# Kernel tuning notes

Measured on AMD Instinct MI355X. Metric: run time of the kernel, lower is better.

The kernel has to match this reference:

```python
import jax, jax.numpy as jnp
import numpy as np

B, ES, HS, NL, NOUT, T = 16384, 64, 64, 3, 2, 128


def setup_inputs() -> dict:
    key = jax.random.key(0)
    ks = jax.random.split(key, 9)
    k = 1.0 / np.sqrt(HS)
    u = lambda kk, shape: jax.random.uniform(kk, shape, jnp.float32, -k, k)
    return {
        "agentFutureTrajEnc": jax.random.normal(ks[0], (B, ES), jnp.float32),
        "emb_w": u(ks[1], (ES, ES)),
        "emb_b": u(ks[2], (ES,)),
        "w_ih": u(ks[3], (NL, 3 * HS, ES)),
        "w_hh": u(ks[4], (NL, 3 * HS, HS)),
        "b_ih": u(ks[5], (NL, 3 * HS)),
        "b_hh": u(ks[6], (NL, 3 * HS)),
        "out_w": u(ks[7], (NOUT, HS)),
        "out_b": u(ks[8], (NOUT,)),
        "target_length": T,
        "batch_size": B,
    }


def _gru_cell(x, h, Wi, Wh, bi, bh):
    # PyTorch GRU cell math: gates ordered (r, z, n)
    gi = x @ Wi.T + bi            # (B, 3*hs)
    gh = h @ Wh.T + bh            # (B, 3*hs)
    ir, iz, inn = jnp.split(gi, 3, axis=-1)
    hr, hz, hn = jnp.split(gh, 3, axis=-1)
    r = jax.nn.sigmoid(ir + hr)
    z = jax.nn.sigmoid(iz + hz)
    n = jnp.tanh(inn + r * hn)
    return (1.0 - z) * n + z * h


def reference(agentFutureTrajEnc, emb_w, emb_b, w_ih, w_hh, b_ih, b_hh, out_w, out_b,
              target_length, batch_size):
    nl = w_ih.shape[0]
    # hidden initialized by repeating the encoding across layers: (nl, B, hs)
    h0 = jnp.broadcast_to(agentFutureTrajEnc[None], (nl,) + agentFutureTrajEnc.shape)

    def step(carry, _):
        x, h = carry                      # x: (B, es), h: (nl, B, hs)
        inp = x @ emb_w.T + emb_b         # embedding Linear(es->es)
        new_h = []
        for l in range(nl):               # small fixed layer loop
            hl = _gru_cell(inp, h[l], w_ih[l], w_hh[l], b_ih[l], b_hh[l])
            new_h.append(hl)
            inp = hl
        h = jnp.stack(new_h)              # (nl, B, hs)
        out = inp @ out_w.T + out_b       # (B, nout)
        return (h[-1], h), out            # next input is top-layer hidden

    _, outs = jax.lax.scan(step, (agentFutureTrajEnc, h0), None, length=target_length)
    return jnp.transpose(outs, (1, 0, 2))  # (B, T, nout)
```

## Files before the change

kernel.cpp:

```cpp
#include <hip/hip_runtime.h>


#define ESZ   64
#define HSZ   64
#define TLEN  128
#define NOUTC 2
#define LDW   72
#define TB16  (16*LDW)
#define L2E   1.44269504f

typedef _Float16 half8 __attribute__((ext_vector_type(8)));
typedef _Float16 half4 __attribute__((ext_vector_type(4)));
typedef float    floatx4 __attribute__((ext_vector_type(4)));
typedef float    floatx2 __attribute__((ext_vector_type(2)));

#define MFMA(a, b, c) __builtin_amdgcn_mfma_f32_16x16x32_f16((a), (b), (c), 0, 0, 0)

__global__ __launch_bounds__(768, 3) void gru_pipe(
    const float* __restrict__ enc,
    const float* __restrict__ emb_w,
    const float* __restrict__ emb_b,
    const float* __restrict__ w_ih,
    const float* __restrict__ w_hh,
    const float* __restrict__ b_ih,
    const float* __restrict__ b_hh,
    const float* __restrict__ out_w,
    const float* __restrict__ out_b,
    float* __restrict__ out)
{
    __shared__ _Float16 s_hl[3 * 4 * 2 * TB16];
    __shared__ float    s_btmp[3 * 64];

    const int tid  = threadIdx.x;
    const int wave = tid >> 6, lane = tid & 63;
    const int l = wave >> 2, g = wave & 3;
    const int q = lane >> 4, c = lane & 15;
    const int u  = (g << 4) | c;
    const int u4 = (g << 4) | (q << 2);
    const long wgbase = (long)blockIdx.x * 64;

    if (tid < 512) {
        const int row = tid >> 3, k0 = (tid & 7) << 3;
        const int j = row >> 4, rr = row & 15;
        const float* p = enc + (wgbase + row) * ESZ + k0;
        floatx4 s0 = *(const floatx4*)p;
        floatx4 s1 = *(const floatx4*)(p + 4);
        half8 v;
        #pragma unroll
        for (int x = 0; x < 4; ++x) { v[x] = (_Float16)s0[x]; v[4 + x] = (_Float16)s1[x]; }
        #pragma unroll
        for (int ly = 0; ly < 3; ++ly)
            *(half8*)&s_hl[((ly * 4 + j) * 2 + 1) * TB16 + rr * LDW + k0] = v;
    }

    auto ldw8s = [&](const float* p, float sc) {
        floatx4 a = *(const floatx4*)p, b = *(const floatx4*)(p + 4);
        half8 v;
        #pragma unroll
        for (int x = 0; x < 4; ++x) { v[x] = (_Float16)(a[x] * sc); v[4 + x] = (_Float16)(b[x] * sc); }
        return v;
    };
    half8 fR[4], fZ[4], fNi[2], fNh[2], fO[2];
    fO[0] = fO[1] = half8{};
    if (l == 0) {
        const float* wi = w_ih;
        const float* wh = w_hh;
        floatx4 aR[4], aZ[4], aN[4];
        #pragma unroll
        for (int x = 0; x < 4; ++x) { aR[x] = {0,0,0,0}; aZ[x] = {0,0,0,0}; aN[x] = {0,0,0,0}; }
        float bR = 0.f, bZ = 0.f, bN = 0.f;
        for (int k4 = 0; k4 < 64; k4 += 4) {
            floatx4 wr4 = *(const floatx4*)(wi + (u) * 64 + k4);
            floatx4 wz4 = *(const floatx4*)(wi + (64 + u) * 64 + k4);
            floatx4 wn4 = *(const floatx4*)(wi + (128 + u) * 64 + k4);
            floatx4 be4 = *(const floatx4*)(emb_b + k4);
            #pragma unroll
            for (int kk = 0; kk < 4; ++kk) {
                const float* er = emb_w + (k4 + kk) * 64;
                floatx4 e0 = *(const floatx4*)(er + q * 8);
                floatx4 e1 = *(const floatx4*)(er + q * 8 + 4);
                floatx4 e2 = *(const floatx4*)(er + 32 + q * 8);
                floatx4 e3 = *(const floatx4*)(er + 32 + q * 8 + 4);
                const float wr = wr4[kk], wz = wz4[kk], wn = wn4[kk];
                aR[0] += wr * e0; aR[1] += wr * e1; aR[2] += wr * e2; aR[3] += wr * e3;
                aZ[0] += wz * e0; aZ[1] += wz * e1; aZ[2] += wz * e2; aZ[3] += wz * e3;
                aN[0] += wn * e0; aN[1] += wn * e1; aN[2] += wn * e2; aN[3] += wn * e3;
                bR += wr * be4[kk]; bZ += wz * be4[kk]; bN += wn * be4[kk];
            }
        }
        #pragma unroll
        for (int x = 0; x < 4; ++x) {
            fR[0][x] = (_Float16)(-L2E * aR[0][x]);   fR[0][4 + x] = (_Float16)(-L2E * aR[1][x]);
            fR[1][x] = (_Float16)(-L2E * aR[2][x]);   fR[1][4 + x] = (_Float16)(-L2E * aR[3][x]);
            fZ[0][x] = (_Float16)(-L2E * aZ[0][x]);   fZ[0][4 + x] = (_Float16)(-L2E * aZ[1][x]);
            fZ[1][x] = (_Float16)(-L2E * aZ[2][x]);   fZ[1][4 + x] = (_Float16)(-L2E * aZ[3][x]);
            fNi[0][x] = (_Float16)(2*L2E * aN[0][x]); fNi[0][4 + x] = (_Float16)(2*L2E * aN[1][x]);
            fNi[1][x] = (_Float16)(2*L2E * aN[2][x]); fNi[1][4 + x] = (_Float16)(2*L2E * aN[3][x]);
        }
        fR[2]  = ldw8s(wh + (u) * 64 + q * 8, -L2E);        fR[3]  = ldw8s(wh + (u) * 64 + 32 + q * 8, -L2E);
        fZ[2]  = ldw8s(wh + (64 + u) * 64 + q * 8, -L2E);   fZ[3]  = ldw8s(wh + (64 + u) * 64 + 32 + q * 8, -L2E);
        fNh[0] = ldw8s(wh + (128 + u) * 64 + q * 8, 2*L2E); fNh[1] = ldw8s(wh + (128 + u) * 64 + 32 + q * 8, 2*L2E);
        if (q == 0) {
            s_btmp[u] = bR; s_btmp[64 + u] = bZ; s_btmp[128 + u] = bN;
        }
        const int oc = (c < NOUTC) ? c : 0;
        fO[0] = ldw8s(out_w + oc * 64 + q * 8, 1.f);
        fO[1] = ldw8s(out_w + oc * 64 + 32 + q * 8, 1.f);
    } else {
        const float* wi = w_ih + l * 3 * HSZ * ESZ;
        const float* wh = w_hh + l * 3 * HSZ * ESZ;
        fR[0]  = ldw8s(wi + (u) * 64 + q * 8, -L2E);        fR[1]  = ldw8s(wi + (u) * 64 + 32 + q * 8, -L2E);
        fR[2]  = ldw8s(wh + (u) * 64 + q * 8, -L2E);        fR[3]  = ldw8s(wh + (u) * 64 + 32 + q * 8, -L2E);
        fZ[0]  = ldw8s(wi + (64 + u) * 64 + q * 8, -L2E);   fZ[1]  = ldw8s(wi + (64 + u) * 64 + 32 + q * 8, -L2E);
        fZ[2]  = ldw8s(wh + (64 + u) * 64 + q * 8, -L2E);   fZ[3]  = ldw8s(wh + (64 + u) * 64 + 32 + q * 8, -L2E);
        fNi[0] = ldw8s(wi + (128 + u) * 64 + q * 8, 2*L2E); fNi[1] = ldw8s(wi + (128 + u) * 64 + 32 + q * 8, 2*L2E);
        fNh[0] = ldw8s(wh + (128 + u) * 64 + q * 8, 2*L2E); fNh[1] = ldw8s(wh + (128 + u) * 64 + 32 + q * 8, 2*L2E);
    }
    __syncthreads();

    floatx4 bR4, bZ4, bNi4, bNh4;
    if (l == 0) {
        #pragma unroll
        for (int i = 0; i < 4; ++i) {
            bR4[i]  = -L2E * (s_btmp[u4 + i] + b_ih[u4 + i] + b_hh[u4 + i]);
            bZ4[i]  = -L2E * (s_btmp[64 + u4 + i] + b_ih[64 + u4 + i] + b_hh[64 + u4 + i]);
            bNi4[i] = 2.f * L2E * (s_btmp[128 + u4 + i] + b_ih[128 + u4 + i]);
            bNh4[i] = 2.f * L2E * b_hh[128 + u4 + i];
        }
    } else {
        const int b0 = l * 192;
        floatx4 bi0 = *(const floatx4*)(b_ih + b0 + u4),       bh0 = *(const floatx4*)(b_hh + b0 + u4);
        floatx4 bi1 = *(const floatx4*)(b_ih + b0 + 64 + u4),  bh1 = *(const floatx4*)(b_hh + b0 + 64 + u4);
        floatx4 bi2 = *(const floatx4*)(b_ih + b0 + 128 + u4), bh2 = *(const floatx4*)(b_hh + b0 + 128 + u4);
        #pragma unroll
        for (int i = 0; i < 4; ++i) {
            bR4[i]  = -L2E * (bi0[i] + bh0[i]);
            bZ4[i]  = -L2E * (bi1[i] + bh1[i]);
            bNi4[i] = 2.f * L2E * bi2[i];
            bNh4[i] = 2.f * L2E * bh2[i];
        }
    }
    const float ob0 = out_b[0], ob1 = out_b[1];

    floatx4 ca0 = *(const floatx4*)(enc + (wgbase +  0 + c) * 64 + u4);
    floatx4 ca1 = *(const floatx4*)(enc + (wgbase + 16 + c) * 64 + u4);
    floatx4 ca2 = *(const floatx4*)(enc + (wgbase + 32 + c) * 64 + u4);
    floatx4 ca3 = *(const floatx4*)(enc + (wgbase + 48 + c) * 64 + u4);

    const int ar = c * LDW + (q << 3);

    auto visit = [&](const int ll, const int j, floatx4& cs, const int t) {
        const int parw = t & 1;
        const _Float16* hb = s_hl + ((ll * 4 + j) * 2 + (parw ^ 1)) * TB16;
        half8 ah0 = *(const half8*)(hb + ar);
        half8 ah1 = *(const half8*)(hb + ar + 32);
        floatx4 accr = bR4, accz = bZ4, accnh = bNh4;
        accr  = MFMA(fR[2], ah0, accr);   accr  = MFMA(fR[3], ah1, accr);
        accz  = MFMA(fZ[2], ah0, accz);   accz  = MFMA(fZ[3], ah1, accz);
        accnh = MFMA(fNh[0], ah0, accnh); accnh = MFMA(fNh[1], ah1, accnh);
        const _Float16* xb = (ll == 0) ? s_hl + ((8 + j) * 2 + (parw ^ 1)) * TB16
                                       : s_hl + (((ll - 1) * 4 + j) * 2 + parw) * TB16;
        half8 bx0 = *(const half8*)(xb + ar);
        half8 bx1 = *(const half8*)(xb + ar + 32);
        accr = MFMA(fR[0], bx0, accr); accr = MFMA(fR[1], bx1, accr);
        accz = MFMA(fZ[0], bx0, accz); accz = MFMA(fZ[1], bx1, accz);
        floatx4 accni = bNi4;
        accni = MFMA(fNi[0], bx0, accni); accni = MFMA(fNi[1], bx1, accni);
        _Float16* hw = s_hl + ((ll * 4 + j) * 2 + parw) * TB16 + c * LDW + u4;
        half4 hv4; floatx4 hnew;
        #pragma unroll
        for (int i = 0; i < 4; ++i) {
            const float r  = __builtin_amdgcn_rcpf(1.f + __builtin_amdgcn_exp2f(accr[i]));
            const float z  = __builtin_amdgcn_rcpf(1.f + __builtin_amdgcn_exp2f(accz[i]));
            const float a  = accni[i] + r * accnh[i];
            const float n  = 1.f - 2.f * __builtin_amdgcn_rcpf(1.f + __builtin_amdgcn_exp2f(a));
            const float hv = n + z * (cs[i] - n);
            hnew[i] = hv; hv4[i] = (_Float16)hv;
        }
        *(half4*)hw = hv4;
        cs = hnew;
        if (ll == 0 && g == j && t >= 1) {
            floatx4 oa = {ob0, ob1, 0.f, 0.f};
            oa = MFMA(fO[0], bx0, oa);
            oa = MFMA(fO[1], bx1, oa);
            if (q == 0) {
                const long row = wgbase + j * 16 + c;
                *(floatx2*)(out + (row * TLEN + (t - 1)) * NOUTC) = floatx2{oa[0], oa[1]};
            }
        }
    };

    for (int s4 = 0; s4 < 129; ++s4) {
        if (l == 0)      { if (s4 < TLEN) visit(0, 0, ca0, s4); }
        else if (l == 1) { if (s4 >= 1)   visit(1, 3, ca3, s4 - 1); }
        else             { if (s4 >= 1)   visit(2, 2, ca2, s4 - 1); }
        __syncthreads();
        if (l == 0)      { if (s4 < TLEN) visit(0, 1, ca1, s4); }
        else if (l == 1) { if (s4 < TLEN) visit(1, 0, ca0, s4); }
        else             { if (s4 >= 1)   visit(2, 3, ca3, s4 - 1); }
        __syncthreads();
        if (l == 0)      { if (s4 < TLEN) visit(0, 2, ca2, s4); }
        else if (l == 1) { if (s4 < TLEN) visit(1, 1, ca1, s4); }
        else             { if (s4 < TLEN) visit(2, 0, ca0, s4); }
        __syncthreads();
        if (l == 0)      { if (s4 < TLEN) visit(0, 3, ca3, s4); }
        else if (l == 1) { if (s4 < TLEN) visit(1, 2, ca2, s4); }
        else             { if (s4 < TLEN) visit(2, 1, ca1, s4); }
        __syncthreads();
    }

    if (l == 0) {
        const _Float16* xb = s_hl + ((8 + g) * 2 + 1) * TB16;
        half8 bx0 = *(const half8*)(xb + ar), bx1 = *(const half8*)(xb + ar + 32);
        floatx4 oa = {ob0, ob1, 0.f, 0.f};
        oa = MFMA(fO[0], bx0, oa);
        oa = MFMA(fO[1], bx1, oa);
        if (q == 0) {
            const long row = wgbase + g * 16 + c;
            *(floatx2*)(out + (row * TLEN + 127) * NOUTC) = floatx2{oa[0], oa[1]};
        }
    }
}

extern "C" void kernel_launch(void* const* d_in, const int* in_sizes, int n_in,
                              void* d_out, int out_size, void* d_ws, size_t ws_size,
                              hipStream_t stream) {
    (void)in_sizes; (void)n_in; (void)d_ws; (void)ws_size; (void)out_size;
    const int grid = 16384 / 64;
    gru_pipe<<<grid, 768, 0, stream>>>(
        (const float*)d_in[0],
        (const float*)d_in[1],
        (const float*)d_in[2],
        (const float*)d_in[3],
        (const float*)d_in[4],
        (const float*)d_in[5],
        (const float*)d_in[6],
        (const float*)d_in[7],
        (const float*)d_in[8],
        (float*)d_out);
}
```

Measured before the change: 459.4 us.

## Halve rows per workgroup and reschedule the layer pipeline into a three-stage wavefront

Each workgroup now handles 32 rows (two 16-row tiles) instead of 64, so the grid doubles to 512 blocks and shared memory per block halves. The per-step schedule becomes a six-phase wavefront over two timesteps, in which layers 0-2 process the two tiles in a staggered order and the output projection gets its own phase. The aim is more workgroups to spread across CUs and a shorter dependency chain per step. Barriers become a raw s_waitcnt lgkmcnt(0) plus s_barrier that skips waiting on global memory, and the sigmoid pair shares one reciprocal. The trade-offs are more barrier phases per timestep, idle wave slots in some phases, and less MFMA work per barrier.

```diff
diff --git a/kernel.cpp b/kernel.cpp
--- a/kernel.cpp
+++ b/kernel.cpp
@@ -15,6 +15,8 @@
 typedef float    floatx2 __attribute__((ext_vector_type(2)));
 
 #define MFMA(a, b, c) __builtin_amdgcn_mfma_f32_16x16x32_f16((a), (b), (c), 0, 0, 0)
+
+#define SBAR() asm volatile("s_waitcnt lgkmcnt(0)\n\ts_barrier" ::: "memory")
 
 __global__ __launch_bounds__(768, 3) void gru_pipe(
     const float* __restrict__ enc,
@@ -28,7 +30,7 @@
     const float* __restrict__ out_b,
     float* __restrict__ out)
 {
-    __shared__ _Float16 s_hl[3 * 4 * 2 * TB16];
+    __shared__ _Float16 s_hl[3 * 2 * 2 * TB16];
     __shared__ float    s_btmp[3 * 64];
 
     const int tid  = threadIdx.x;
@@ -37,9 +39,9 @@
     const int q = lane >> 4, c = lane & 15;
     const int u  = (g << 4) | c;
     const int u4 = (g << 4) | (q << 2);
-    const long wgbase = (long)blockIdx.x * 64;
-
-    if (tid < 512) {
+    const long wgbase = (long)blockIdx.x * 32;
+
+    if (tid < 256) {
         const int row = tid >> 3, k0 = (tid & 7) << 3;
         const int j = row >> 4, rr = row & 15;
         const float* p = enc + (wgbase + row) * ESZ + k0;
@@ -50,7 +52,7 @@
         for (int x = 0; x < 4; ++x) { v[x] = (_Float16)s0[x]; v[4 + x] = (_Float16)s1[x]; }
         #pragma unroll
         for (int ly = 0; ly < 3; ++ly)
-            *(half8*)&s_hl[((ly * 4 + j) * 2 + 1) * TB16 + rr * LDW + k0] = v;
+            *(half8*)&s_hl[((ly * 2 + j) * 2 + 1) * TB16 + rr * LDW + k0] = v;
     }
 
     auto ldw8s = [&](const float* p, float sc) {
@@ -144,89 +146,93 @@
 
     floatx4 ca0 = *(const floatx4*)(enc + (wgbase +  0 + c) * 64 + u4);
     floatx4 ca1 = *(const floatx4*)(enc + (wgbase + 16 + c) * 64 + u4);
-    floatx4 ca2 = *(const floatx4*)(enc + (wgbase + 32 + c) * 64 + u4);
-    floatx4 ca3 = *(const floatx4*)(enc + (wgbase + 48 + c) * 64 + u4);
 
     const int ar = c * LDW + (q << 3);
 
-    auto visit = [&](const int ll, const int j, floatx4& cs, const int t) {
-        const int parw = t & 1;
-        const _Float16* hb = s_hl + ((ll * 4 + j) * 2 + (parw ^ 1)) * TB16;
+    auto visit = [&](const int ll, const int j, floatx4& cs, const int t,
+                     const int parw) {
+        const _Float16* hb = s_hl + ((ll * 2 + j) * 2 + (parw ^ 1)) * TB16;
+        const _Float16* xb = (ll == 0) ? s_hl + ((4 + j) * 2 + (parw ^ 1)) * TB16
+                                       : s_hl + (((ll - 1) * 2 + j) * 2 + parw) * TB16;
         half8 ah0 = *(const half8*)(hb + ar);
         half8 ah1 = *(const half8*)(hb + ar + 32);
+        half8 bx0 = *(const half8*)(xb + ar);
+        half8 bx1 = *(const half8*)(xb + ar + 32);
         floatx4 accr = bR4, accz = bZ4, accnh = bNh4;
         accr  = MFMA(fR[2], ah0, accr);   accr  = MFMA(fR[3], ah1, accr);
         accz  = MFMA(fZ[2], ah0, accz);   accz  = MFMA(fZ[3], ah1, accz);
         accnh = MFMA(fNh[0], ah0, accnh); accnh = MFMA(fNh[1], ah1, accnh);
-        const _Float16* xb = (ll == 0) ? s_hl + ((8 + j) * 2 + (parw ^ 1)) * TB16
-                                       : s_hl + (((ll - 1) * 4 + j) * 2 + parw) * TB16;
-        half8 bx0 = *(const half8*)(xb + ar);
-        half8 bx1 = *(const half8*)(xb + ar + 32);
         accr = MFMA(fR[0], bx0, accr); accr = MFMA(fR[1], bx1, accr);
         accz = MFMA(fZ[0], bx0, accz); accz = MFMA(fZ[1], bx1, accz);
         floatx4 accni = bNi4;
         accni = MFMA(fNi[0], bx0, accni); accni = MFMA(fNi[1], bx1, accni);
-        _Float16* hw = s_hl + ((ll * 4 + j) * 2 + parw) * TB16 + c * LDW + u4;
+        _Float16* hw = s_hl + ((ll * 2 + j) * 2 + parw) * TB16 + c * LDW + u4;
         half4 hv4; floatx4 hnew;
         #pragma unroll
         for (int i = 0; i < 4; ++i) {
-            const float r  = __builtin_amdgcn_rcpf(1.f + __builtin_amdgcn_exp2f(accr[i]));
-            const float z  = __builtin_amdgcn_rcpf(1.f + __builtin_amdgcn_exp2f(accz[i]));
-            const float a  = accni[i] + r * accnh[i];
+            const float er = __builtin_amdgcn_exp2f(accr[i]);
+            const float ez = __builtin_amdgcn_exp2f(accz[i]);
+            const float pr = 1.f + er, pz = 1.f + ez;
+            const float qq = __builtin_amdgcn_rcpf(pr * pz);
+            const float rr = qq * pz;
+            const float zz = qq * pr;
+            const float a  = accni[i] + rr * accnh[i];
             const float n  = 1.f - 2.f * __builtin_amdgcn_rcpf(1.f + __builtin_amdgcn_exp2f(a));
-            const float hv = n + z * (cs[i] - n);
+            const float hv = n + zz * (cs[i] - n);
             hnew[i] = hv; hv4[i] = (_Float16)hv;
         }
         *(half4*)hw = hv4;
         cs = hnew;
-        if (ll == 0 && g == j && t >= 1) {
-            floatx4 oa = {ob0, ob1, 0.f, 0.f};
-            oa = MFMA(fO[0], bx0, oa);
-            oa = MFMA(fO[1], bx1, oa);
-            if (q == 0) {
-                const long row = wgbase + j * 16 + c;
-                *(floatx2*)(out + (row * TLEN + (t - 1)) * NOUTC) = floatx2{oa[0], oa[1]};
-            }
-        }
     };
 
-    for (int s4 = 0; s4 < 129; ++s4) {
-        if (l == 0)      { if (s4 < TLEN) visit(0, 0, ca0, s4); }
-        else if (l == 1) { if (s4 >= 1)   visit(1, 3, ca3, s4 - 1); }
-        else             { if (s4 >= 1)   visit(2, 2, ca2, s4 - 1); }
-        __syncthreads();
-        if (l == 0)      { if (s4 < TLEN) visit(0, 1, ca1, s4); }
-        else if (l == 1) { if (s4 < TLEN) visit(1, 0, ca0, s4); }
-        else             { if (s4 >= 1)   visit(2, 3, ca3, s4 - 1); }
-        __syncthreads();
-        if (l == 0)      { if (s4 < TLEN) visit(0, 2, ca2, s4); }
-        else if (l == 1) { if (s4 < TLEN) visit(1, 1, ca1, s4); }
-        else             { if (s4 < TLEN) visit(2, 0, ca0, s4); }
-        __syncthreads();
-        if (l == 0)      { if (s4 < TLEN) visit(0, 3, ca3, s4); }
-        else if (l == 1) { if (s4 < TLEN) visit(1, 2, ca2, s4); }
-        else             { if (s4 < TLEN) visit(2, 1, ca1, s4); }
-        __syncthreads();
-    }
-
-    if (l == 0) {
-        const _Float16* xb = s_hl + ((8 + g) * 2 + 1) * TB16;
-        half8 bx0 = *(const half8*)(xb + ar), bx1 = *(const half8*)(xb + ar + 32);
+    auto visO = [&](const int j, const int t, const int par) {
+        const _Float16* xb = s_hl + ((4 + j) * 2 + par) * TB16;
+        half8 b0 = *(const half8*)(xb + ar);
+        half8 b1 = *(const half8*)(xb + ar + 32);
         floatx4 oa = {ob0, ob1, 0.f, 0.f};
-        oa = MFMA(fO[0], bx0, oa);
-        oa = MFMA(fO[1], bx1, oa);
+        oa = MFMA(fO[0], b0, oa);
+        oa = MFMA(fO[1], b1, oa);
         if (q == 0) {
-            const long row = wgbase + g * 16 + c;
-            *(floatx2*)(out + (row * TLEN + 127) * NOUTC) = floatx2{oa[0], oa[1]};
-        }
-    }
+            const long row = wgbase + j * 16 + c;
+            *(floatx2*)(out + (row * TLEN + t) * NOUTC) = floatx2{oa[0], oa[1]};
+        }
+    };
+
+    for (int t = 0; t < TLEN; t += 2) {
+        const bool vv = (t != 0);
+        if (l == 0)      visit(0, 0, ca0, t, 0);
+        else if (l == 2) { if (vv) visit(2, 1, ca1, t - 1, 1); }
+        SBAR();
+        if (l == 0)      visit(0, 1, ca1, t, 0);
+        else if (l == 1) visit(1, 0, ca0, t, 0);
+        SBAR();
+        if (l == 0)      { if (vv && g < 2) visO(g, t - 1, 1); }
+        else if (l == 1) visit(1, 1, ca1, t, 0);
+        else             visit(2, 0, ca0, t, 0);
+        SBAR();
+        if (l == 0)      visit(0, 0, ca0, t + 1, 1);
+        else if (l == 2) visit(2, 1, ca1, t, 0);
+        SBAR();
+        if (l == 0)      visit(0, 1, ca1, t + 1, 1);
+        else if (l == 1) visit(1, 0, ca0, t + 1, 1);
+        SBAR();
+        if (l == 0)      { if (g < 2) visO(g, t, 0); }
+        else if (l == 1) visit(1, 1, ca1, t + 1, 1);
+        else             visit(2, 0, ca0, t + 1, 1);
+        SBAR();
+    }
+
+    if (l == 2)           visit(2, 1, ca1, TLEN - 1, 1);
+    else if (l == 0 && g == 0) visO(0, TLEN - 1, 1);
+    SBAR();
+    if (l == 0 && g == 1) visO(1, TLEN - 1, 1);
 }
 
 extern "C" void kernel_launch(void* const* d_in, const int* in_sizes, int n_in,
                               void* d_out, int out_size, void* d_ws, size_t ws_size,
                               hipStream_t stream) {
     (void)in_sizes; (void)n_in; (void)d_ws; (void)ws_size; (void)out_size;
-    const int grid = 16384 / 64;
+    const int grid = 16384 / 32;
     gru_pipe<<<grid, 768, 0, stream>>>(
         (const float*)d_in[0],
         (const float*)d_in[1],
```

After: 547.3 us. +19.1%, slower.
